# Kernel optimization log

Hardware: AMD Instinct MI355X
Metric: run time of the kernel (lower is better)

Reference implementation:

```python
import jax, jax.numpy as jnp
import numpy as np
from jax import lax

DIM = 384
NUM_HEADS = 8
KV_NUM_HEADS = 2
REP = NUM_HEADS // KV_NUM_HEADS  # 4
KV_DIM = DIM * 2 // REP          # 192
EPS_LN = 1e-5
EPS_NORM = 1e-12


def _layernorm_channel(x, w, b):
    # WithBias LayerNorm over channel dim of NCHW tensor (matches to_3d -> LN(c) -> to_4d)
    mu = jnp.mean(x, axis=1, keepdims=True)
    var = jnp.var(x, axis=1, keepdims=True)
    return (x - mu) / jnp.sqrt(var + EPS_LN) * w[None, :, None, None] + b[None, :, None, None]


def _conv1x1(x, w):
    # w: [out, in] ; x: [b, in, h, w]
    return jnp.einsum('oi,bihw->bohw', w, x)


def _dwconv3x3(x, w):
    # depthwise 3x3, padding=1; w: [C, 1, 3, 3]
    C = x.shape[1]
    return lax.conv_general_dilated(
        x, w, window_strides=(1, 1), padding=((1, 1), (1, 1)),
        feature_group_count=C,
        dimension_numbers=('NCHW', 'OIHW', 'NCHW'))


def _l2norm(x):
    n = jnp.linalg.norm(x, axis=-1, keepdims=True)
    return x / jnp.maximum(n, EPS_NORM)


def setup_inputs() -> dict:
    key = jax.random.key(0)
    ks = jax.random.split(key, 8)
    b, h, w = 8, 128, 128
    scale1 = 1.0 / np.sqrt(DIM)
    return {
        'q': jax.random.normal(ks[0], (b, DIM, h, w), dtype=jnp.float32),
        'k': jax.random.normal(ks[1], (b, DIM, h, w), dtype=jnp.float32),
        'w_q': jax.random.normal(ks[2], (DIM, DIM), dtype=jnp.float32) * scale1,
        'w_kv': jax.random.normal(ks[3], (KV_DIM, DIM), dtype=jnp.float32) * scale1,
        'w_q_dw': jax.random.normal(ks[4], (DIM, 1, 3, 3), dtype=jnp.float32) * (1.0 / 3.0),
        'w_kv_dw': jax.random.normal(ks[5], (KV_DIM, 1, 3, 3), dtype=jnp.float32) * (1.0 / 3.0),
        'w_out': jax.random.normal(ks[6], (DIM, DIM), dtype=jnp.float32) * scale1,
        'temperature': jnp.ones((NUM_HEADS, 1, 1), dtype=jnp.float32),
        'lnq_w': jnp.ones((DIM,), dtype=jnp.float32),
        'lnq_b': jnp.zeros((DIM,), dtype=jnp.float32),
        'lnk_w': jnp.ones((DIM,), dtype=jnp.float32),
        'lnk_b': jnp.zeros((DIM,), dtype=jnp.float32),
    }


def reference(q, k, w_q, w_kv, w_q_dw, w_kv_dw, w_out, temperature,
              lnq_w, lnq_b, lnk_w, lnk_b):
    b, c, h, w = q.shape
    hw = h * w
    qn = _layernorm_channel(q, lnq_w, lnq_b)
    kn = _layernorm_channel(k, lnk_w, lnk_b)
    qp = _dwconv3x3(_conv1x1(qn, w_q), w_q_dw)          # [b, dim, h, w]
    kv = _dwconv3x3(_conv1x1(kn, w_kv), w_kv_dw)        # [b, 2*dim/rep, h, w]
    kk, vv = jnp.split(kv, 2, axis=1)                   # each [b, dim/rep, h, w]
    # reshape to heads: channel-attention layout [b, head, c_head, hw]
    qh = qp.reshape(b, NUM_HEADS, DIM // NUM_HEADS, hw)
    kh = kk.reshape(b, KV_NUM_HEADS, DIM // NUM_HEADS, hw)
    vh = vv.reshape(b, KV_NUM_HEADS, DIM // NUM_HEADS, hw)
    # GQA repeat kv heads (repeat_interleave on head dim)
    kh = jnp.repeat(kh, REP, axis=1)
    vh = jnp.repeat(vh, REP, axis=1)
    qh = _l2norm(qh)
    kh = _l2norm(kh)
    attn = jnp.einsum('bhck,bhdk->bhcd', qh, kh) * temperature[None]
    attn = jax.nn.softmax(attn, axis=-1)
    out = jnp.einsum('bhcd,bhdk->bhck', attn, vh)       # [b, head, c_head, hw]
    out = out.reshape(b, DIM, h, w)
    return _conv1x1(out, w_out)
```

## Files before the change

### kernel.cpp

```cpp
#include <hip/hip_runtime.h>
#include <math.h>


typedef unsigned short u16;
typedef unsigned int u32;
typedef short s16x8 __attribute__((ext_vector_type(8)));
typedef float f32x4 __attribute__((ext_vector_type(4)));

#define HW 16384
#define NB 8
#define CDIM 384
#define KVC 192

__device__ __forceinline__ float b2f(u16 u) {
  return __uint_as_float(((u32)u) << 16);
}
__device__ __forceinline__ u16 f2b(float f) {
  u32 u = __float_as_uint(f);
  u += 0x7fffu + ((u >> 16) & 1u);
  return (u16)(u >> 16);
}
__device__ __forceinline__ u32 pack2(float a, float c) {
  return (u32)f2b(a) | ((u32)f2b(c) << 16);
}

__global__ void k0_prep(const float* __restrict__ wq, const float* __restrict__ wkv,
                        const float* __restrict__ wo,
                        const float* __restrict__ lnqw, const float* __restrict__ lnqb,
                        const float* __restrict__ lnkw, const float* __restrict__ lnkb,
                        u16* __restrict__ wqp, float* __restrict__ rwsQ, float* __restrict__ biasQ,
                        u16* __restrict__ wkvp, float* __restrict__ rwsKV, float* __restrict__ biasKV,
                        u16* __restrict__ wop) {
  int r = blockIdx.x * 256 + threadIdx.x;
  if (r < 384) {
    float rs = 0.f, bs = 0.f;
    for (int i = 0; i < 384; ++i) {
      float wp = wq[r * 384 + i] * lnqw[i];
      u16 h = f2b(wp);
      rs += b2f(h);
      bs += wq[r * 384 + i] * lnqb[i];
      wqp[r * 384 + i] = h;
    }
    rwsQ[r] = rs; biasQ[r] = bs;
  } else if (r < 768) {
    int o = r - 384;
    if (o < 192) {
      float rs = 0.f, bs = 0.f;
      for (int i = 0; i < 384; ++i) {
        float wp = wkv[o * 384 + i] * lnkw[i];
        u16 h = f2b(wp);
        rs += b2f(h);
        bs += wkv[o * 384 + i] * lnkb[i];
        wkvp[o * 384 + i] = h;
      }
      rwsKV[o] = rs; biasKV[o] = bs;
    } else {
      for (int i = 0; i < 384; ++i) wkvp[o * 384 + i] = 0;
      rwsKV[o] = 0.f; biasKV[o] = 0.f;
    }
  } else if (r < 1152) {
    int o = r - 768;
    for (int i = 0; i < 384; ++i) wop[o * 384 + i] = f2b(wo[o * 384 + i]);
  }
}

template <int MODE, int WM, int WN, int MF, int NF>
__global__ __launch_bounds__(512, 4) void gemm_fused(const u16* __restrict__ A,
                                                     const void* __restrict__ Bsrc,
                                                     const float* __restrict__ rowsum,
                                                     const float* __restrict__ bias,
                                                     void* __restrict__ outv, int M) {
  __shared__ __align__(16) char smem[57344];
  u16*   tB    = (u16*)smem;
  float* sredS = (float*)(smem + 49152);
  float* sredQ = (float*)(smem + 53248);
  u16*   chB16 = (u16*)smem;
  __shared__ float muL[64], sdL[64];

  constexpr int M_TILE = WM * MF * 16;

  const int b = blockIdx.z;
  const int pt = ((blockIdx.x & 7) << 5) | (blockIdx.x >> 3);
  const int tid = threadIdx.x;
  const int w = tid >> 6, l = tid & 63;
  const int wm = (WN == 1) ? w : (w >> 1);
  const int wn = (WN == 1) ? 0 : (w & 1);
  const int lr = l & 15, lg = l >> 4;

  f32x4 acc[MF][NF] = {};

  {
    const float* Bf = (const float*)Bsrc;
    const size_t fbase = (size_t)b * CDIM * HW + (size_t)pt * 64 + l;
    float v[48];
#pragma unroll
    for (int it = 0; it < 12; ++it)
#pragma unroll
      for (int j = 0; j < 4; ++j)
        v[it * 4 + j] = Bf[fbase + (size_t)(it * 32 + w * 4 + j) * HW];

    float s_ = 0.f, q_ = 0.f;
#pragma unroll
    for (int it = 0; it < 12; ++it) {
      float v0 = v[it * 4], v1 = v[it * 4 + 1], v2 = v[it * 4 + 2], v3 = v[it * 4 + 3];
      s_ += (v0 + v1) + (v2 + v3);
      q_ += (v0 * v0 + v1 * v1) + (v2 * v2 + v3 * v3);
      u32 lo = pack2(v0, v1), hi = pack2(v2, v3);
      int cidx = it * 4 + (w >> 1);
      int off = l * 384 + ((cidx ^ (l & 7)) << 3) + (w & 1) * 4;
      *(uint2*)&tB[off] = make_uint2(lo, hi);
    }
    sredS[w * 64 + l] = s_;
    sredQ[w * 64 + l] = q_;
  }
  __syncthreads();

  if (tid < 64) {
    float s = 0.f, q2 = 0.f;
#pragma unroll
    for (int g = 0; g < 8; ++g) { s += sredS[g * 64 + tid]; q2 += sredQ[g * 64 + tid]; }
    float mn = s * (1.f / 384.f);
    float var = q2 * (1.f / 384.f) - mn * mn;
    muL[tid] = mn;
    sdL[tid] = rsqrtf(var + 1e-5f);
  }
  __syncthreads();

  s16x8 a[2][MF], bb[2][NF];
#pragma unroll
  for (int mf = 0; mf < MF; ++mf)
    a[0][mf] = *(const s16x8*)(A + (size_t)(wm * (MF * 16) + mf * 16 + lr) * 384 + lg * 8);
#pragma unroll
  for (int nf = 0; nf < NF; ++nf) {
    int row = wn * (NF * 16) + nf * 16 + lr;
    bb[0][nf] = *(const s16x8*)&tB[row * 384 + ((lg ^ (row & 7)) << 3)];
  }
#pragma unroll
  for (int ks = 0; ks < 12; ++ks) {
    const int cur = ks & 1, nxt = cur ^ 1;
    if (ks < 11) {
      const int ko = (ks + 1) * 32 + lg * 8;
      const int cidx = (ks + 1) * 4 + lg;
#pragma unroll
      for (int mf = 0; mf < MF; ++mf)
        a[nxt][mf] = *(const s16x8*)(A + (size_t)(wm * (MF * 16) + mf * 16 + lr) * 384 + ko);
#pragma unroll
      for (int nf = 0; nf < NF; ++nf) {
        int row = wn * (NF * 16) + nf * 16 + lr;
        bb[nxt][nf] = *(const s16x8*)&tB[row * 384 + ((cidx ^ (row & 7)) << 3)];
      }
    }
#pragma unroll
    for (int mf = 0; mf < MF; ++mf)
#pragma unroll
      for (int nf = 0; nf < NF; ++nf)
        acc[mf][nf] = __builtin_amdgcn_mfma_f32_16x16x32_bf16(a[cur][mf], bb[cur][nf], acc[mf][nf], 0, 0, 0);
  }

  __syncthreads();
#pragma unroll
  for (int nf = 0; nf < NF; ++nf) {
    int prow = wn * (NF * 16) + nf * 16 + lr;
    float m_ = muL[prow], s_ = sdL[prow];
#pragma unroll
    for (int mf = 0; mf < MF; ++mf)
#pragma unroll
      for (int r = 0; r < 4; ++r) {
        int orow = wm * (MF * 16) + mf * 16 + lg * 4 + r;
        float v = s_ * (acc[mf][nf][r] - m_ * rowsum[orow]) + bias[orow];
        chB16[orow * 72 + prow] = f2b(v);
      }
  }
  __syncthreads();
  const int total = M_TILE * 8;
  for (int i = tid; i < total; i += 512) {
    int row = i >> 3, c8 = i & 7;
    if (row < M) {
      uint4 v = *(const uint4*)&chB16[row * 72 + c8 * 8];
      *(uint4*)((u16*)outv + ((size_t)(b * M + row)) * HW + pt * 64 + c8 * 8) = v;
    }
  }
}

__global__ __launch_bounds__(256) void k4_dw(const u16* __restrict__ qp, const u16* __restrict__ kvp,
                                             const float* __restrict__ wqdw, const float* __restrict__ wkvdw,
                                             u16* __restrict__ qd, u16* __restrict__ kvd,
                                             float* __restrict__ rnq, float* __restrict__ rnk) {
  __shared__ u16 plane[16384];
  __shared__ float red[256];

  int c = blockIdx.x, b = blockIdx.y;
  int tid = threadIdx.x;
  const u16* in; u16* outb; const float* wp; int C;
  int isQ = (c < 384), cc = isQ ? c : c - 384;
  if (isQ) { in = qp; outb = qd; wp = wqdw + cc * 9; C = CDIM; }
  else     { in = kvp; outb = kvd; wp = wkvdw + cc * 9; C = KVC; }
  size_t base = ((size_t)(b * C + cc)) * HW;

  float w[9];
#pragma unroll
  for (int j = 0; j < 9; ++j) w[j] = wp[j];

  const uint4* gsrc = (const uint4*)(in + base);
  uint4* lplane = (uint4*)plane;
#pragma unroll
  for (int i = 0; i < 8; ++i) lplane[tid + i * 256] = gsrc[tid + i * 256];
  __syncthreads();

  uint4* gdst = (uint4*)(outb + base);
  float ns = 0.f;
#pragma unroll
  for (int it = 0; it < 8; ++it) {
    int idx = tid + it * 256;
    int y = idx >> 4, ox = idx & 15;
    int x0 = ox * 8;

    float r[3][10];
#pragma unroll
    for (int rr = 0; rr < 3; ++rr) {
      int yy = y + rr - 1;
      if ((unsigned)yy < 128u) {
        int rbase = yy * 128 + x0;
        r[rr][0] = (x0 > 0) ? b2f(plane[rbase - 1]) : 0.f;
        uint4 v = *(const uint4*)&plane[rbase];
        u32 ws[4] = {v.x, v.y, v.z, v.w};
#pragma unroll
        for (int j = 0; j < 4; ++j) {
          r[rr][1 + 2 * j] = b2f((u16)(ws[j] & 0xffff));
          r[rr][2 + 2 * j] = b2f((u16)(ws[j] >> 16));
        }
        r[rr][9] = (x0 < 120) ? b2f(plane[rbase + 8]) : 0.f;
      } else {
#pragma unroll
        for (int j = 0; j < 10; ++j) r[rr][j] = 0.f;
      }
    }

    u32 packed[4];
#pragma unroll
    for (int j = 0; j < 8; ++j) {
      float a = 0.f;
#pragma unroll
      for (int rr = 0; rr < 3; ++rr)
#pragma unroll
        for (int dx = 0; dx < 3; ++dx)
          a += w[rr * 3 + dx] * r[rr][j + dx];
      u16 h = f2b(a);
      float hv = b2f(h);
      ns += hv * hv;
      if (j & 1) packed[j >> 1] |= ((u32)h) << 16; else packed[j >> 1] = (u32)h;
    }
    gdst[idx] = make_uint4(packed[0], packed[1], packed[2], packed[3]);
  }

  red[tid] = ns;
  __syncthreads();
  for (int st = 128; st > 0; st >>= 1) {
    if (tid < st) red[tid] += red[tid + st];
    __syncthreads();
  }
  if (tid == 0) {
    float n = sqrtf(red[0]);
    float inv = 1.f / fmaxf(n, 1e-12f);
    if (isQ) rnq[b * 384 + cc] = inv;
    else if (cc < 96) rnk[b * 96 + cc] = inv;
  }
}

__global__ void k5b_vt(const u16* __restrict__ kvd, u16* __restrict__ vt) {
  int p = blockIdx.x * 256 + threadIdx.x;
  int b = blockIdx.y;
  size_t sb = ((size_t)(b * KVC + 96)) * HW + p;
  uint4* dv = (uint4*)vt + ((size_t)(b * HW + p)) * 12;
  for (int j8 = 0; j8 < 12; ++j8) {
    u32 w[4];
#pragma unroll
    for (int j = 0; j < 8; ++j) {
      u16 h = kvd[sb + (size_t)(j8 * 8 + j) * HW];
      if (j & 1) w[j >> 1] |= ((u32)h) << 16; else w[j >> 1] = (u32)h;
    }
    dv[j8] = make_uint4(w[0], w[1], w[2], w[3]);
  }
}

__global__ __launch_bounds__(256) void k6_qk(const u16* __restrict__ qd,
                                             const u16* __restrict__ kvd,
                                             float* __restrict__ spart) {
  int kc = blockIdx.x, h = blockIdx.y, b = blockIdx.z;
  int tid = threadIdx.x;
  int w = tid >> 6, l = tid & 63, lr = l & 15, lg = l >> 4;
  int g = h >> 2;
  int p0 = kc * 2048 + w * 512;

  f32x4 acc[3][3] = {};
  size_t qbase = ((size_t)(b * CDIM + h * 48 + lr)) * HW;
  size_t kbase = ((size_t)(b * KVC + g * 48 + lr)) * HW;

  for (int ks = 0; ks < 16; ++ks) {
    int pp = p0 + ks * 32 + lg * 8;
    s16x8 a[3], bb[3];
#pragma unroll
    for (int mi = 0; mi < 3; ++mi) a[mi] = *(const s16x8*)(qd + qbase + (size_t)mi * 16 * HW + pp);
#pragma unroll
    for (int ni = 0; ni < 3; ++ni) bb[ni] = *(const s16x8*)(kvd + kbase + (size_t)ni * 16 * HW + pp);
#pragma unroll
    for (int mi = 0; mi < 3; ++mi)
#pragma unroll
      for (int ni = 0; ni < 3; ++ni)
        acc[mi][ni] = __builtin_amdgcn_mfma_f32_16x16x32_bf16(a[mi], bb[ni], acc[mi][ni], 0, 0, 0);
  }

  size_t sb = ((size_t)((((b * 8 + h) * 8) + kc) * 4 + w)) * 2304;
#pragma unroll
  for (int mi = 0; mi < 3; ++mi)
#pragma unroll
    for (int ni = 0; ni < 3; ++ni)
#pragma unroll
      for (int r = 0; r < 4; ++r) {
        int c = mi * 16 + lg * 4 + r, d = ni * 16 + lr;
        spart[sb + c * 48 + d] = acc[mi][ni][r];
      }
}

__global__ void k7_sm(const float* __restrict__ spart, const float* __restrict__ temp,
                      const float* __restrict__ rnq, const float* __restrict__ rnk,
                      u16* __restrict__ ptil) {
  int h = blockIdx.x, b = blockIdx.y, tid = threadIdx.x;
  int g = h >> 2;
  __shared__ float S[2304];
  size_t base = ((size_t)((b * 8 + h) * 32)) * 2304;
  for (int e = tid; e < 2304; e += 64) {
    float s = 0.f;
    for (int j = 0; j < 32; ++j) s += spart[base + (size_t)j * 2304 + e];
    S[e] = s;
  }
  __syncthreads();
  if (tid < 48) {
    int c = tid;
    float sq = temp[h] * rnq[b * 384 + h * 48 + c];
    float mx = -1e30f;
    for (int d = 0; d < 48; ++d) {
      float v = S[c * 48 + d] * sq * rnk[b * 96 + g * 48 + d];
      mx = fmaxf(mx, v);
    }
    float sum = 0.f;
    for (int d = 0; d < 48; ++d) {
      float v = S[c * 48 + d] * sq * rnk[b * 96 + g * 48 + d];
      sum += __expf(v - mx);
    }
    float inv = 1.f / sum;
    u16* row = ptil + ((size_t)(b * 384 + h * 48 + c)) * 96;
    for (int dk = 0; dk < 96; ++dk) {
      int d = dk - g * 48;
      float pv = 0.f;
      if (d >= 0 && d < 48) {
        float v = S[c * 48 + d] * sq * rnk[b * 96 + g * 48 + d];
        pv = __expf(v - mx) * inv;
      }
      row[dk] = f2b(pv);
    }
  }
}

__global__ __launch_bounds__(1024, 4) void k8_out(const u16* __restrict__ vt,
                                                  const u16* __restrict__ ptil,
                                                  const u16* __restrict__ wop,
                                                  float* __restrict__ out) {
  __shared__ __align__(16) char smem[125952];
  u16* tB = (u16*)smem;
  u16* tV = (u16*)(smem + 98304);
  float* chB32 = (float*)smem;

  const int b = blockIdx.z;
  const int pt = ((blockIdx.x & 7) << 4) | (blockIdx.x >> 3);
  const int tid = threadIdx.x;
  const int w = tid >> 6, l = tid & 63;
  const int wm = w >> 1, wn = w & 1;
  const int lr = l & 15, lg = l >> 4;

  {
#pragma unroll
    for (int i = 0; i < 2; ++i) {
      int c0 = tid + i * 1024;
      if (c0 < 1536) {
        int row = c0 / 12, cc = c0 % 12;
        uint4 v = *(const uint4*)(vt + ((size_t)(b * HW + pt * 128 + row)) * 96 + cc * 8);
        *(uint4*)&tV[row * 104 + cc * 8] = v;
      }
    }
  }
  __syncthreads();

  {
    f32x4 accA[3][4] = {};
#pragma unroll
    for (int ks = 0; ks < 3; ++ks) {
      s16x8 a[3], bb[4];
#pragma unroll
      for (int mf = 0; mf < 3; ++mf)
        a[mf] = *(const s16x8*)(ptil + ((size_t)(b * 384 + wm * 48 + mf * 16 + lr)) * 96 + ks * 32 + lg * 8);
#pragma unroll
      for (int nf = 0; nf < 4; ++nf)
        bb[nf] = *(const s16x8*)&tV[(wn * 64 + nf * 16 + lr) * 104 + ks * 32 + lg * 8];
#pragma unroll
      for (int mf = 0; mf < 3; ++mf)
#pragma unroll
        for (int nf = 0; nf < 4; ++nf)
          accA[mf][nf] = __builtin_amdgcn_mfma_f32_16x16x32_bf16(a[mf], bb[nf], accA[mf][nf], 0, 0, 0);
    }
#pragma unroll
    for (int mf = 0; mf < 3; ++mf)
#pragma unroll
      for (int nf = 0; nf < 4; ++nf) {
        int prow = wn * 64 + nf * 16 + lr;
        int cbase = wm * 48 + mf * 16 + lg * 4;
        u32 lo = pack2(accA[mf][nf][0], accA[mf][nf][1]);
        u32 hi = pack2(accA[mf][nf][2], accA[mf][nf][3]);
        int chunk = (cbase >> 3) ^ ((prow >> 1) & 7);
        int off = prow * 384 + chunk * 8 + (cbase & 7);
        *(uint2*)&tB[off] = make_uint2(lo, hi);
      }
  }
  __syncthreads();

  f32x4 acc[3][4] = {};
  {
    s16x8 a[2][3], bb[2][4];
#pragma unroll
    for (int mf = 0; mf < 3; ++mf)
      a[0][mf] = *(const s16x8*)(wop + (size_t)(wm * 48 + mf * 16 + lr) * 384 + lg * 8);
#pragma unroll
    for (int nf = 0; nf < 4; ++nf) {
      int row = wn * 64 + nf * 16 + lr;
      bb[0][nf] = *(const s16x8*)&tB[row * 384 + ((lg ^ ((row >> 1) & 7)) << 3)];
    }
#pragma unroll
    for (int ks = 0; ks < 12; ++ks) {
      const int cur = ks & 1, nxt = cur ^ 1;
      if (ks < 11) {
        const int ko = (ks + 1) * 32 + lg * 8;
        const int cidx = (ks + 1) * 4 + lg;
#pragma unroll
        for (int mf = 0; mf < 3; ++mf)
          a[nxt][mf] = *(const s16x8*)(wop + (size_t)(wm * 48 + mf * 16 + lr) * 384 + ko);
#pragma unroll
        for (int nf = 0; nf < 4; ++nf) {
          int row = wn * 64 + nf * 16 + lr;
          bb[nxt][nf] = *(const s16x8*)&tB[row * 384 + ((cidx ^ ((row >> 1) & 7)) << 3)];
        }
      }
#pragma unroll
      for (int mf = 0; mf < 3; ++mf)
#pragma unroll
        for (int nf = 0; nf < 4; ++nf)
          acc[mf][nf] = __builtin_amdgcn_mfma_f32_16x16x32_bf16(a[cur][mf], bb[cur][nf], acc[mf][nf], 0, 0, 0);
    }
  }

#pragma unroll
  for (int cc = 0; cc < 2; ++cc) {
    __syncthreads();
    if ((wm >> 2) == cc) {
#pragma unroll
      for (int nf = 0; nf < 4; ++nf) {
        int prow = wn * 64 + nf * 16 + lr;
#pragma unroll
        for (int mf = 0; mf < 3; ++mf)
#pragma unroll
          for (int r = 0; r < 4; ++r) {
            int orow_l = (wm & 3) * 48 + mf * 16 + lg * 4 + r;
            chB32[orow_l * 132 + prow] = acc[mf][nf][r];
          }
      }
    }
    __syncthreads();
    for (int i = tid; i < 192 * 32; i += 1024) {
      int row = i >> 5, c4 = i & 31;
      uint4 v = *(const uint4*)&chB32[row * 132 + c4 * 4];
      *(uint4*)(out + ((size_t)(b * CDIM + cc * 192 + row)) * HW + pt * 128 + c4 * 4) = v;
    }
  }
}

extern "C" void kernel_launch(void* const* d_in, const int* in_sizes, int n_in,
                              void* d_out, int out_size, void* d_ws, size_t ws_size,
                              hipStream_t stream) {
  const float* q    = (const float*)d_in[0];
  const float* k    = (const float*)d_in[1];
  const float* w_q  = (const float*)d_in[2];
  const float* w_kv = (const float*)d_in[3];
  const float* w_qd = (const float*)d_in[4];
  const float* w_kd = (const float*)d_in[5];
  const float* w_o  = (const float*)d_in[6];
  const float* temp = (const float*)d_in[7];
  const float* lnqw = (const float*)d_in[8];
  const float* lnqb = (const float*)d_in[9];
  const float* lnkw = (const float*)d_in[10];
  const float* lnkb = (const float*)d_in[11];
  float* out = (float*)d_out;

  char* ws = (char*)d_ws;
  size_t off = 0;
  auto alloc = [&](size_t bytes) -> void* {
    void* p = ws + off;
    off += (bytes + 255) & ~(size_t)255;
    return p;
  };

  u16*   wqp   = (u16*)alloc(384 * 384 * 2);
  float* rwsQ  = (float*)alloc(384 * 4);
  float* biasQ = (float*)alloc(384 * 4);
  u16*   wkvp  = (u16*)alloc(384 * 384 * 2);
  float* rwsKV = (float*)alloc(384 * 4);
  float* biasKV= (float*)alloc(384 * 4);
  u16*   wop   = (u16*)alloc(384 * 384 * 2);
  u16*   qp    = (u16*)alloc((size_t)NB * CDIM * HW * 2);
  u16*   kvp   = (u16*)alloc((size_t)NB * KVC * HW * 2);
  u16*   qd    = (u16*)alloc((size_t)NB * CDIM * HW * 2);
  u16*   kvd   = (u16*)alloc((size_t)NB * KVC * HW * 2);
  u16*   vt    = (u16*)alloc((size_t)NB * HW * 96 * 2);
  float* spart = (float*)alloc((size_t)2048 * 2304 * 4);
  u16*   ptil  = (u16*)alloc((size_t)NB * CDIM * 96 * 2);
  float* rnq   = (float*)alloc((size_t)NB * 384 * 4);
  float* rnk   = (float*)alloc((size_t)NB * 96 * 4);

  k0_prep<<<5, 256, 0, stream>>>(w_q, w_kv, w_o, lnqw, lnqb, lnkw, lnkb,
                                 wqp, rwsQ, biasQ, wkvp, rwsKV, biasKV, wop);

  gemm_fused<0, 8, 1, 3, 4><<<dim3(256, 1, NB), 512, 0, stream>>>(wqp, q, rwsQ, biasQ, qp, 384);
  gemm_fused<0, 4, 2, 3, 2><<<dim3(256, 1, NB), 512, 0, stream>>>(wkvp, k, rwsKV, biasKV, kvp, 192);

  k4_dw<<<dim3(576, NB), 256, 0, stream>>>(qp, kvp, w_qd, w_kd, qd, kvd, rnq, rnk);

  k5b_vt<<<dim3(64, NB), 256, 0, stream>>>(kvd, vt);

  k6_qk<<<dim3(8, 8, NB), 256, 0, stream>>>(qd, kvd, spart);
  k7_sm<<<dim3(8, NB), 64, 0, stream>>>(spart, temp, rnq, rnk, ptil);

  k8_out<<<dim3(128, 1, NB), 1024, 0, stream>>>(vt, ptil, wop, out);
}
```

Before: 546.2 us.

## Widen projection GEMM tile to 128 pixels with 1024-thread blocks

Replaces the templated projection GEMM with a single kernel that handles 128 pixels per block using 16 waves, loading float2 per lane and computing LayerNorm stats for two pixels per thread. The epilogue is staged in two 192-row halves through shared memory. The KV projection now uses the same 384-row tiling with zero-padded weights, so it does wasted MFMA work on the padded rows. Larger tiles improve weight reuse and memory coalescing but need about 113KB of LDS, which limits occupancy to one block per CU.

```diff
diff --git a/kernel.cpp b/kernel.cpp
--- a/kernel.cpp
+++ b/kernel.cpp
@@ -64,61 +64,60 @@
   }
 }
 
-template <int MODE, int WM, int WN, int MF, int NF>
-__global__ __launch_bounds__(512, 4) void gemm_fused(const u16* __restrict__ A,
-                                                     const void* __restrict__ Bsrc,
+__global__ __launch_bounds__(1024, 4) void gemm_proj(const u16* __restrict__ A,
+                                                     const float* __restrict__ Bf,
                                                      const float* __restrict__ rowsum,
                                                      const float* __restrict__ bias,
-                                                     void* __restrict__ outv, int M) {
-  __shared__ __align__(16) char smem[57344];
-  u16*   tB    = (u16*)smem;
-  float* sredS = (float*)(smem + 49152);
-  float* sredQ = (float*)(smem + 53248);
-  u16*   chB16 = (u16*)smem;
-  __shared__ float muL[64], sdL[64];
-
-  constexpr int M_TILE = WM * MF * 16;
+                                                     u16* __restrict__ outp, int M) {
+  __shared__ __align__(16) char smem[115712];
+  u16*    tB   = (u16*)smem;
+  float2* sred = (float2*)(smem + 98304);
+  float*  muL  = (float*)(smem + 114688);
+  float*  sdL  = (float*)(smem + 115200);
+  u16*    chB16 = (u16*)smem;
 
   const int b = blockIdx.z;
-  const int pt = ((blockIdx.x & 7) << 5) | (blockIdx.x >> 3);
+  const int pt = ((blockIdx.x & 7) << 4) | (blockIdx.x >> 3);
   const int tid = threadIdx.x;
   const int w = tid >> 6, l = tid & 63;
-  const int wm = (WN == 1) ? w : (w >> 1);
-  const int wn = (WN == 1) ? 0 : (w & 1);
+  const int wm = w >> 1, wn = w & 1;
   const int lr = l & 15, lg = l >> 4;
 
-  f32x4 acc[MF][NF] = {};
+  f32x4 acc[3][4] = {};
 
   {
-    const float* Bf = (const float*)Bsrc;
-    const size_t fbase = (size_t)b * CDIM * HW + (size_t)pt * 64 + l;
-    float v[48];
-#pragma unroll
-    for (int it = 0; it < 12; ++it)
-#pragma unroll
-      for (int j = 0; j < 4; ++j)
-        v[it * 4 + j] = Bf[fbase + (size_t)(it * 32 + w * 4 + j) * HW];
-
-    float s_ = 0.f, q_ = 0.f;
-#pragma unroll
-    for (int it = 0; it < 12; ++it) {
-      float v0 = v[it * 4], v1 = v[it * 4 + 1], v2 = v[it * 4 + 2], v3 = v[it * 4 + 3];
-      s_ += (v0 + v1) + (v2 + v3);
-      q_ += (v0 * v0 + v1 * v1) + (v2 * v2 + v3 * v3);
-      u32 lo = pack2(v0, v1), hi = pack2(v2, v3);
-      int cidx = it * 4 + (w >> 1);
-      int off = l * 384 + ((cidx ^ (l & 7)) << 3) + (w & 1) * 4;
-      *(uint2*)&tB[off] = make_uint2(lo, hi);
-    }
-    sredS[w * 64 + l] = s_;
-    sredQ[w * 64 + l] = q_;
-  }
-  __syncthreads();
-
-  if (tid < 64) {
+    const float* src = Bf + (size_t)b * CDIM * HW + (size_t)pt * 128 + 2 * l;
+    float2 v[24];
+#pragma unroll
+    for (int j = 0; j < 24; ++j)
+      v[j] = *(const float2*)(src + (size_t)(w * 24 + j) * HW);
+
+    float s0 = 0.f, q0 = 0.f, s1 = 0.f, q1 = 0.f;
+    const int p0r = 2 * l, p1r = 2 * l + 1;
+#pragma unroll
+    for (int j4 = 0; j4 < 6; ++j4) {
+      float2 v0 = v[j4 * 4], v1 = v[j4 * 4 + 1], v2 = v[j4 * 4 + 2], v3 = v[j4 * 4 + 3];
+      s0 += (v0.x + v1.x) + (v2.x + v3.x);
+      q0 += (v0.x * v0.x + v1.x * v1.x) + (v2.x * v2.x + v3.x * v3.x);
+      s1 += (v0.y + v1.y) + (v2.y + v3.y);
+      q1 += (v0.y * v0.y + v1.y * v1.y) + (v2.y * v2.y + v3.y * v3.y);
+      int cbase = w * 24 + j4 * 4;
+      int cidx = cbase >> 3;
+      int sub = cbase & 7;
+      *(uint2*)&tB[p0r * 384 + ((cidx ^ (p0r & 7)) << 3) + sub] =
+          make_uint2(pack2(v0.x, v1.x), pack2(v2.x, v3.x));
+      *(uint2*)&tB[p1r * 384 + ((cidx ^ (p1r & 7)) << 3) + sub] =
+          make_uint2(pack2(v0.y, v1.y), pack2(v2.y, v3.y));
+    }
+    sred[w * 128 + p0r] = make_float2(s0, q0);
+    sred[w * 128 + p1r] = make_float2(s1, q1);
+  }
+  __syncthreads();
+
+  if (tid < 128) {
     float s = 0.f, q2 = 0.f;
 #pragma unroll
-    for (int g = 0; g < 8; ++g) { s += sredS[g * 64 + tid]; q2 += sredQ[g * 64 + tid]; }
+    for (int g = 0; g < 16; ++g) { float2 t = sred[g * 128 + tid]; s += t.x; q2 += t.y; }
     float mn = s * (1.f / 384.f);
     float var = q2 * (1.f / 384.f) - mn * mn;
     muL[tid] = mn;
@@ -126,13 +125,13 @@
   }
   __syncthreads();
 
-  s16x8 a[2][MF], bb[2][NF];
-#pragma unroll
-  for (int mf = 0; mf < MF; ++mf)
-    a[0][mf] = *(const s16x8*)(A + (size_t)(wm * (MF * 16) + mf * 16 + lr) * 384 + lg * 8);
-#pragma unroll
-  for (int nf = 0; nf < NF; ++nf) {
-    int row = wn * (NF * 16) + nf * 16 + lr;
+  s16x8 a[2][3], bb[2][4];
+#pragma unroll
+  for (int mf = 0; mf < 3; ++mf)
+    a[0][mf] = *(const s16x8*)(A + (size_t)(wm * 48 + mf * 16 + lr) * 384 + lg * 8);
+#pragma unroll
+  for (int nf = 0; nf < 4; ++nf) {
+    int row = wn * 64 + nf * 16 + lr;
     bb[0][nf] = *(const s16x8*)&tB[row * 384 + ((lg ^ (row & 7)) << 3)];
   }
 #pragma unroll
@@ -142,42 +141,47 @@
       const int ko = (ks + 1) * 32 + lg * 8;
       const int cidx = (ks + 1) * 4 + lg;
 #pragma unroll
-      for (int mf = 0; mf < MF; ++mf)
-        a[nxt][mf] = *(const s16x8*)(A + (size_t)(wm * (MF * 16) + mf * 16 + lr) * 384 + ko);
-#pragma unroll
-      for (int nf = 0; nf < NF; ++nf) {
-        int row = wn * (NF * 16) + nf * 16 + lr;
+      for (int mf = 0; mf < 3; ++mf)
+        a[nxt][mf] = *(const s16x8*)(A + (size_t)(wm * 48 + mf * 16 + lr) * 384 + ko);
+#pragma unroll
+      for (int nf = 0; nf < 4; ++nf) {
+        int row = wn * 64 + nf * 16 + lr;
         bb[nxt][nf] = *(const s16x8*)&tB[row * 384 + ((cidx ^ (row & 7)) << 3)];
       }
     }
 #pragma unroll
-    for (int mf = 0; mf < MF; ++mf)
-#pragma unroll
-      for (int nf = 0; nf < NF; ++nf)
+    for (int mf = 0; mf < 3; ++mf)
+#pragma unroll
+      for (int nf = 0; nf < 4; ++nf)
         acc[mf][nf] = __builtin_amdgcn_mfma_f32_16x16x32_bf16(a[cur][mf], bb[cur][nf], acc[mf][nf], 0, 0, 0);
   }
 
-  __syncthreads();
-#pragma unroll
-  for (int nf = 0; nf < NF; ++nf) {
-    int prow = wn * (NF * 16) + nf * 16 + lr;
-    float m_ = muL[prow], s_ = sdL[prow];
-#pragma unroll
-    for (int mf = 0; mf < MF; ++mf)
-#pragma unroll
-      for (int r = 0; r < 4; ++r) {
-        int orow = wm * (MF * 16) + mf * 16 + lg * 4 + r;
-        float v = s_ * (acc[mf][nf][r] - m_ * rowsum[orow]) + bias[orow];
-        chB16[orow * 72 + prow] = f2b(v);
-      }
-  }
-  __syncthreads();
-  const int total = M_TILE * 8;
-  for (int i = tid; i < total; i += 512) {
-    int row = i >> 3, c8 = i & 7;
-    if (row < M) {
-      uint4 v = *(const uint4*)&chB16[row * 72 + c8 * 8];
-      *(uint4*)((u16*)outv + ((size_t)(b * M + row)) * HW + pt * 64 + c8 * 8) = v;
+#pragma unroll
+  for (int cc = 0; cc < 2; ++cc) {
+    __syncthreads();
+    if ((wm >> 2) == cc) {
+#pragma unroll
+      for (int nf = 0; nf < 4; ++nf) {
+        int prow = wn * 64 + nf * 16 + lr;
+        float m_ = muL[prow], s_ = sdL[prow];
+#pragma unroll
+        for (int mf = 0; mf < 3; ++mf)
+#pragma unroll
+          for (int r = 0; r < 4; ++r) {
+            int orow = wm * 48 + mf * 16 + lg * 4 + r;
+            float vv = s_ * (acc[mf][nf][r] - m_ * rowsum[orow]) + bias[orow];
+            chB16[((wm & 3) * 48 + mf * 16 + lg * 4 + r) * 136 + prow] = f2b(vv);
+          }
+      }
+    }
+    __syncthreads();
+    for (int i = tid; i < 192 * 16; i += 1024) {
+      int row = i >> 4, c8 = i & 15;
+      int g = cc * 192 + row;
+      if (g < M) {
+        uint4 v = *(const uint4*)&chB16[row * 136 + c8 * 8];
+        *(uint4*)(outp + ((size_t)(b * M + g)) * HW + pt * 128 + c8 * 8) = v;
+      }
     }
   }
 }
@@ -527,8 +531,8 @@
   k0_prep<<<5, 256, 0, stream>>>(w_q, w_kv, w_o, lnqw, lnqb, lnkw, lnkb,
                                  wqp, rwsQ, biasQ, wkvp, rwsKV, biasKV, wop);
 
-  gemm_fused<0, 8, 1, 3, 4><<<dim3(256, 1, NB), 512, 0, stream>>>(wqp, q, rwsQ, biasQ, qp, 384);
-  gemm_fused<0, 4, 2, 3, 2><<<dim3(256, 1, NB), 512, 0, stream>>>(wkvp, k, rwsKV, biasKV, kvp, 192);
+  gemm_proj<<<dim3(128, 1, NB), 1024, 0, stream>>>(wqp, q, rwsQ, biasQ, qp, 384);
+  gemm_proj<<<dim3(128, 1, NB), 1024, 0, stream>>>(wkvp, k, rwsKV, biasKV, kvp, 192);
 
   k4_dw<<<dim3(576, NB), 256, 0, stream>>>(qp, kvp, w_qd, w_kd, qd, kvd, rnq, rnk);
 
```

Result: slower. 595.6 us (+9.0%).
